# Kernel optimization log

Hardware: AMD Instinct MI355X
Metric: run time of the kernel (lower is better)

Reference implementation:

```python
import jax, jax.numpy as jnp
import numpy as np

N = 100000          # nodes
MUL = 64            # multiplicity of each irrep in input_1 (64x0e + 64x1o)
O0, O1M, O2M = 320, 128, 64   # output multiplicities: 320x0e + 128x1o + 64x1e
SQRT3 = float(np.sqrt(3.0))
SQRT6 = float(np.sqrt(6.0))
# e3nn path weights: sqrt(dim(ir_out) / sum_paths_to_out(mul1*mul2))
PW0 = float(1.0 / np.sqrt(2.0 * MUL))     # 0e: two paths, x = 128
PW1 = float(np.sqrt(3.0 / (2.0 * MUL)))   # 1o: two paths, x = 128
PW2 = float(np.sqrt(3.0 / MUL))           # 1e: one path,  x = 64


def setup_inputs() -> dict:
    key = jax.random.key(0)
    k = jax.random.split(key, 8)
    return {
        "input_1": jax.random.normal(k[0], (N, 4 * MUL), jnp.float32),  # 64x0e + 64x1o
        "input_2": jax.random.normal(k[1], (N, 4), jnp.float32),        # 1x0e + 1x1o
        "W_a0_o0": jax.random.normal(k[2], (MUL, O0), jnp.float32),     # 0e x 0e -> 0e
        "W_b1_o0": jax.random.normal(k[3], (MUL, O0), jnp.float32),     # 1o x 1o -> 0e
        "W_a1_o1": jax.random.normal(k[4], (MUL, O1M), jnp.float32),    # 0e x 1o -> 1o
        "W_b0_o1": jax.random.normal(k[5], (MUL, O1M), jnp.float32),    # 1o x 0e -> 1o
        "W_b1_o2": jax.random.normal(k[6], (MUL, O2M), jnp.float32),    # 1o x 1o -> 1e
        "bias": jnp.zeros((O0,), jnp.float32),                          # on the 0e scalars
    }


def reference(input_1, input_2, W_a0_o0, W_b1_o0, W_a1_o1, W_b0_o1, W_b1_o2, bias):
    n = input_1.shape[0]
    s_a = input_1[:, :MUL]                        # [N, MUL]      0e block
    v_b = input_1[:, MUL:].reshape(n, MUL, 3)     # [N, MUL, 3]   1o block
    s0 = input_2[:, :1]                           # [N, 1]        0e attr
    v1 = input_2[:, 1:]                           # [N, 3]        1o attr

    # --- 0e output: (0e*0e) and (1o.1o)/sqrt3 (CG delta_ij/sqrt3), fully-connected weights
    dot_b1 = jnp.einsum('nuk,nk->nu', v_b, v1)    # [N, MUL]
    o0 = PW0 * ((s_a * s0) @ W_a0_o0 + (dot_b1 / SQRT3) @ W_b1_o0) + bias  # [N, O0]

    # --- 1o output: (0e x 1o) and (1o x 0e), CG delta/sqrt3
    o1 = (PW1 / SQRT3) * (
        jnp.einsum('nu,uw->nw', s_a, W_a1_o1)[:, :, None] * v1[:, None, :]
        + jnp.einsum('nuk,uw->nwk', v_b, W_b0_o1) * s0[:, :, None]
    )                                             # [N, O1M, 3]

    # --- 1e output: (1o x 1o), CG eps_ijk/sqrt6 -> cross product
    cr = jnp.cross(v_b, v1[:, None, :])           # [N, MUL, 3]
    o2 = (PW2 / SQRT6) * jnp.einsum('nuk,uw->nwk', cr, W_b1_o2)  # [N, O2M, 3]

    return jnp.concatenate([o0, o1.reshape(n, -1), o2.reshape(n, -1)], axis=-1)  # [N, 896]
```

## Files before the change

kernel.cpp:

```cpp
#include <hip/hip_runtime.h>


typedef __bf16 v8bf __attribute__((ext_vector_type(8)));
typedef float f32x4 __attribute__((ext_vector_type(4)));

#define PW0f   0.08838834764831845f
#define PW0S3f 0.05103103630798288f


__global__ __launch_bounds__(256) void prep_weights(
    const float* __restrict__ Wa0, const float* __restrict__ Wb1o0,
    const float* __restrict__ Wa1, const float* __restrict__ Wb0,
    const float* __restrict__ Wo2, unsigned short* __restrict__ ws) {
  int t = blockIdx.x * 256 + threadIdx.x;
  float v;
  int k, n, KS, base;
  if (t < 40960) {
    k = t / 320; n = t % 320; KS = 4; base = 0;
    v = (k < 64) ? Wa0[k * 320 + n] * PW0f : Wb1o0[(k - 64) * 320 + n] * PW0S3f;
  } else if (t < 49152) {
    int tt = t - 40960; k = tt / 128; n = tt % 128; KS = 2; base = 40960;
    v = Wa1[k * 128 + n] * PW0f;
  } else if (t < 57344) {
    int tt = t - 49152; k = tt / 128; n = tt % 128; KS = 2; base = 49152;
    v = Wb0[k * 128 + n] * PW0f;
  } else if (t < 61440) {
    int tt = t - 57344; k = tt / 64; n = tt % 64; KS = 2; base = 57344;
    v = Wo2[k * 64 + n] * PW0f;
  } else {
    return;
  }
  int nt = n >> 4, cc = n & 15, ks = k >> 5, qq = (k >> 3) & 3, j = k & 7;
  int addr = base + ((nt * KS + ks) * 64 + qq * 16 + cc) * 8 + j;
  __bf16 h = (__bf16)v;
  ws[addr] = __builtin_bit_cast(unsigned short, h);
}

__device__ __forceinline__ int fidx(int k, int m) {
  return (((k >> 5) * 64 + ((k >> 3) & 3) * 16 + m) * 8) + (k & 7);
}

__global__ __launch_bounds__(256) void tp_main(
    const float* __restrict__ in1, const float* __restrict__ in2,
    const float* __restrict__ bias, const unsigned short* __restrict__ wsb,
    float* __restrict__ out, int N) {
  __shared__ __attribute__((aligned(16))) float raw[16 * 256];
  __shared__ __attribute__((aligned(16))) float s0v1[16 * 4];
  __shared__ __attribute__((aligned(16))) __bf16 f0[2048];
  __shared__ __attribute__((aligned(16))) __bf16 fsa[1024];
  __shared__ __attribute__((aligned(16))) __bf16 fvb[3][1024];
  __shared__ __attribute__((aligned(16))) __bf16 fcr[3][1024];

  const int tid = threadIdx.x;
  const int r0 = blockIdx.x * 16;

  if (tid < 64) {
    int m = tid >> 2, cmp = tid & 3;
    int rr = r0 + m; if (rr >= N) rr = N - 1;
    s0v1[tid] = in2[rr * 4 + cmp];
  }
  for (int i = tid; i < 1024; i += 256) {
    int row = i >> 6, c4 = i & 63;
    int rr = r0 + row; if (rr >= N) rr = N - 1;
    const float4 v = *(const float4*)(in1 + (size_t)rr * 256 + c4 * 4);
    *(float4*)(raw + row * 256 + c4 * 4) = v;
  }
  __syncthreads();

  {
    const int m = tid >> 4;
    const float s0  = s0v1[m * 4 + 0];
    const float v1x = s0v1[m * 4 + 1];
    const float v1y = s0v1[m * 4 + 2];
    const float v1z = s0v1[m * 4 + 3];
#pragma unroll
    for (int du = 0; du < 4; ++du) {
      const int u = (tid & 15) * 4 + du;
      const float sa = raw[m * 256 + u];
      const float b0 = raw[m * 256 + 64 + 3 * u + 0];
      const float b1 = raw[m * 256 + 64 + 3 * u + 1];
      const float b2 = raw[m * 256 + 64 + 3 * u + 2];
      f0[fidx(u, m)]      = (__bf16)(sa * s0);
      f0[fidx(64 + u, m)] = (__bf16)(b0 * v1x + b1 * v1y + b2 * v1z);
      fsa[fidx(u, m)]     = (__bf16)sa;
      fvb[0][fidx(u, m)]  = (__bf16)b0;
      fvb[1][fidx(u, m)]  = (__bf16)b1;
      fvb[2][fidx(u, m)]  = (__bf16)b2;
      fcr[0][fidx(u, m)]  = (__bf16)(b1 * v1z - b2 * v1y);
      fcr[1][fidx(u, m)]  = (__bf16)(b2 * v1x - b0 * v1z);
      fcr[2][fidx(u, m)]  = (__bf16)(b0 * v1y - b1 * v1x);
    }
  }
  __syncthreads();

  const int lane = tid & 63;
  const int wv = tid >> 6;
  const int c = lane & 15, q = lane >> 4;

  const unsigned short* B0p = wsb;
  const unsigned short* Ba1 = wsb + 40960;
  const unsigned short* Bb0 = wsb + 49152;
  const unsigned short* Bo2 = wsb + 57344;

  for (int job = wv; job < 32; job += 4) {
    if (job < 20) {
      const int nt = job;
      f32x4 acc = {0.f, 0.f, 0.f, 0.f};
#pragma unroll
      for (int ks = 0; ks < 4; ++ks) {
        v8bf a = *(const v8bf*)(f0 + (ks * 64 + lane) * 8);
        v8bf b = *(const v8bf*)(B0p + ((nt * 4 + ks) * 64 + lane) * 8);
        acc = __builtin_amdgcn_mfma_f32_16x16x32_bf16(a, b, acc, 0, 0, 0);
      }
      const int col = nt * 16 + c;
      const float bv = bias[col];
#pragma unroll
      for (int r = 0; r < 4; ++r) {
        const int row = r0 + q * 4 + r;
        if (row < N) out[(size_t)row * 896 + col] = acc[r] + bv;
      }
    } else if (job < 28) {
      const int jt = job - 20;
      f32x4 t1 = {0.f, 0.f, 0.f, 0.f};
      f32x4 t2[3];
      t2[0] = t1; t2[1] = t1; t2[2] = t1;
      v8bf ba0 = *(const v8bf*)(Ba1 + ((jt * 2 + 0) * 64 + lane) * 8);
      v8bf ba1 = *(const v8bf*)(Ba1 + ((jt * 2 + 1) * 64 + lane) * 8);
      v8bf bb0 = *(const v8bf*)(Bb0 + ((jt * 2 + 0) * 64 + lane) * 8);
      v8bf bb1 = *(const v8bf*)(Bb0 + ((jt * 2 + 1) * 64 + lane) * 8);
      {
        v8bf a0 = *(const v8bf*)(fsa + (0 * 64 + lane) * 8);
        v8bf a1 = *(const v8bf*)(fsa + (1 * 64 + lane) * 8);
        t1 = __builtin_amdgcn_mfma_f32_16x16x32_bf16(a0, ba0, t1, 0, 0, 0);
        t1 = __builtin_amdgcn_mfma_f32_16x16x32_bf16(a1, ba1, t1, 0, 0, 0);
      }
#pragma unroll
      for (int k = 0; k < 3; ++k) {
        v8bf a0 = *(const v8bf*)(fvb[k] + (0 * 64 + lane) * 8);
        v8bf a1 = *(const v8bf*)(fvb[k] + (1 * 64 + lane) * 8);
        t2[k] = __builtin_amdgcn_mfma_f32_16x16x32_bf16(a0, bb0, t2[k], 0, 0, 0);
        t2[k] = __builtin_amdgcn_mfma_f32_16x16x32_bf16(a1, bb1, t2[k], 0, 0, 0);
      }
#pragma unroll
      for (int r = 0; r < 4; ++r) {
        const int row = q * 4 + r;
        const int gr = r0 + row;
        if (gr < N) {
          const float s0  = s0v1[row * 4 + 0];
          const float v1x = s0v1[row * 4 + 1];
          const float v1y = s0v1[row * 4 + 2];
          const float v1z = s0v1[row * 4 + 3];
          const size_t base = (size_t)gr * 896 + 320 + 3 * (jt * 16 + c);
          out[base + 0] = t1[r] * v1x + t2[0][r] * s0;
          out[base + 1] = t1[r] * v1y + t2[1][r] * s0;
          out[base + 2] = t1[r] * v1z + t2[2][r] * s0;
        }
      }
    } else {
      const int jt = job - 28;
      f32x4 ac[3];
      ac[0] = f32x4{0.f, 0.f, 0.f, 0.f}; ac[1] = ac[0]; ac[2] = ac[0];
      v8bf b0v = *(const v8bf*)(Bo2 + ((jt * 2 + 0) * 64 + lane) * 8);
      v8bf b1v = *(const v8bf*)(Bo2 + ((jt * 2 + 1) * 64 + lane) * 8);
#pragma unroll
      for (int k = 0; k < 3; ++k) {
        v8bf a0 = *(const v8bf*)(fcr[k] + (0 * 64 + lane) * 8);
        v8bf a1 = *(const v8bf*)(fcr[k] + (1 * 64 + lane) * 8);
        ac[k] = __builtin_amdgcn_mfma_f32_16x16x32_bf16(a0, b0v, ac[k], 0, 0, 0);
        ac[k] = __builtin_amdgcn_mfma_f32_16x16x32_bf16(a1, b1v, ac[k], 0, 0, 0);
      }
#pragma unroll
      for (int r = 0; r < 4; ++r) {
        const int row = q * 4 + r;
        const int gr = r0 + row;
        if (gr < N) {
          const size_t base = (size_t)gr * 896 + 704 + 3 * (jt * 16 + c);
          out[base + 0] = ac[0][r];
          out[base + 1] = ac[1][r];
          out[base + 2] = ac[2][r];
        }
      }
    }
  }
}

extern "C" void kernel_launch(void* const* d_in, const int* in_sizes, int n_in,
                              void* d_out, int out_size, void* d_ws, size_t ws_size,
                              hipStream_t stream) {
  const float* in1   = (const float*)d_in[0];
  const float* in2   = (const float*)d_in[1];
  const float* Wa0   = (const float*)d_in[2];
  const float* Wb1o0 = (const float*)d_in[3];
  const float* Wa1   = (const float*)d_in[4];
  const float* Wb0   = (const float*)d_in[5];
  const float* Wo2   = (const float*)d_in[6];
  const float* bias  = (const float*)d_in[7];
  float* out = (float*)d_out;
  unsigned short* ws = (unsigned short*)d_ws;

  const int N = in_sizes[0] / 256;

  hipLaunchKernelGGL(prep_weights, dim3(240), dim3(256), 0, stream,
                     Wa0, Wb1o0, Wa1, Wb0, Wo2, ws);
  const int nblocks = (N + 15) / 16;
  hipLaunchKernelGGL(tp_main, dim3(nblocks), dim3(256), 0, stream,
                     in1, in2, bias, ws, out, N);
}
```

Measured before the change: 469.7 us.

## Apply per-row attribute scalars after MFMA instead of building product features

The per-row scalars (s0, v1) are factored out of the matmuls, so the MFMAs run directly on raw sa and vb features and the dot, cross and scale are applied to the accumulators in the epilogue. This removes the staging buffer of raw fp32 input and the f0/fcr feature arrays from shared memory, and the global loads now feed bf16 packing directly as vector stores. A-operand fragments are loaded into registers once and reused across all jobs, and launch bounds request higher occupancy. In exchange, the 0e output path needs more MFMAs (4 accumulators instead of 1), and the epilogue does more FLOPs.

```diff
diff --git a/kernel.cpp b/kernel.cpp
--- a/kernel.cpp
+++ b/kernel.cpp
@@ -2,6 +2,7 @@
 
 
 typedef __bf16 v8bf __attribute__((ext_vector_type(8)));
+typedef __bf16 v4bf __attribute__((ext_vector_type(4)));
 typedef float f32x4 __attribute__((ext_vector_type(4)));
 
 #define PW0f   0.08838834764831845f
@@ -13,82 +14,59 @@
     const float* __restrict__ Wa1, const float* __restrict__ Wb0,
     const float* __restrict__ Wo2, unsigned short* __restrict__ ws) {
   int t = blockIdx.x * 256 + threadIdx.x;
-  float v;
-  int k, n, KS, base;
-  if (t < 40960) {
-    k = t / 320; n = t % 320; KS = 4; base = 0;
-    v = (k < 64) ? Wa0[k * 320 + n] * PW0f : Wb1o0[(k - 64) * 320 + n] * PW0S3f;
+  float v; int k, n, base;
+  if (t < 20480) {
+    k = t / 320; n = t % 320; base = 0;     v = Wa0[k * 320 + n] * PW0f;
+  } else if (t < 40960) {
+    int tt = t - 20480; k = tt / 320; n = tt % 320; base = 20480; v = Wb1o0[k * 320 + n] * PW0S3f;
   } else if (t < 49152) {
-    int tt = t - 40960; k = tt / 128; n = tt % 128; KS = 2; base = 40960;
-    v = Wa1[k * 128 + n] * PW0f;
+    int tt = t - 40960; k = tt / 128; n = tt % 128; base = 40960; v = Wa1[k * 128 + n] * PW0f;
   } else if (t < 57344) {
-    int tt = t - 49152; k = tt / 128; n = tt % 128; KS = 2; base = 49152;
-    v = Wb0[k * 128 + n] * PW0f;
-  } else if (t < 61440) {
-    int tt = t - 57344; k = tt / 64; n = tt % 64; KS = 2; base = 57344;
-    v = Wo2[k * 64 + n] * PW0f;
+    int tt = t - 49152; k = tt / 128; n = tt % 128; base = 49152; v = Wb0[k * 128 + n] * PW0f;
   } else {
-    return;
+    int tt = t - 57344; k = tt / 64;  n = tt % 64;  base = 57344; v = Wo2[k * 64 + n] * PW0f;
   }
   int nt = n >> 4, cc = n & 15, ks = k >> 5, qq = (k >> 3) & 3, j = k & 7;
-  int addr = base + ((nt * KS + ks) * 64 + qq * 16 + cc) * 8 + j;
+  int addr = base + ((nt * 2 + ks) * 64 + qq * 16 + cc) * 8 + j;
   __bf16 h = (__bf16)v;
   ws[addr] = __builtin_bit_cast(unsigned short, h);
 }
 
-__device__ __forceinline__ int fidx(int k, int m) {
-  return (((k >> 5) * 64 + ((k >> 3) & 3) * 16 + m) * 8) + (k & 7);
-}
-
-__global__ __launch_bounds__(256) void tp_main(
+__global__ __launch_bounds__(256, 4) void tp_main(
     const float* __restrict__ in1, const float* __restrict__ in2,
     const float* __restrict__ bias, const unsigned short* __restrict__ wsb,
     float* __restrict__ out, int N) {
-  __shared__ __attribute__((aligned(16))) float raw[16 * 256];
   __shared__ __attribute__((aligned(16))) float s0v1[16 * 4];
-  __shared__ __attribute__((aligned(16))) __bf16 f0[2048];
   __shared__ __attribute__((aligned(16))) __bf16 fsa[1024];
   __shared__ __attribute__((aligned(16))) __bf16 fvb[3][1024];
-  __shared__ __attribute__((aligned(16))) __bf16 fcr[3][1024];
 
   const int tid = threadIdx.x;
   const int r0 = blockIdx.x * 16;
 
-  if (tid < 64) {
-    int m = tid >> 2, cmp = tid & 3;
+  {
+    const int m = tid & 15;
+    const int g = tid >> 4;
     int rr = r0 + m; if (rr >= N) rr = N - 1;
-    s0v1[tid] = in2[rr * 4 + cmp];
-  }
-  for (int i = tid; i < 1024; i += 256) {
-    int row = i >> 6, c4 = i & 63;
-    int rr = r0 + row; if (rr >= N) rr = N - 1;
-    const float4 v = *(const float4*)(in1 + (size_t)rr * 256 + c4 * 4);
-    *(float4*)(raw + row * 256 + c4 * 4) = v;
-  }
-  __syncthreads();
-
-  {
-    const int m = tid >> 4;
-    const float s0  = s0v1[m * 4 + 0];
-    const float v1x = s0v1[m * 4 + 1];
-    const float v1y = s0v1[m * 4 + 2];
-    const float v1z = s0v1[m * 4 + 3];
+    const float* rp = in1 + (size_t)rr * 256;
+    const float4 sa4 = *(const float4*)(rp + 4 * g);
+    const float4 w0  = *(const float4*)(rp + 64 + 12 * g);
+    const float4 w1  = *(const float4*)(rp + 64 + 12 * g + 4);
+    const float4 w2  = *(const float4*)(rp + 64 + 12 * g + 8);
+    const float vf[12] = {w0.x, w0.y, w0.z, w0.w, w1.x, w1.y, w1.z, w1.w,
+                          w2.x, w2.y, w2.z, w2.w};
+    const int wbase = (((g >> 3) * 64 + ((g >> 1) & 3) * 16 + m) * 8) + 4 * (g & 1);
+    v4bf pk;
+    pk[0] = (__bf16)sa4.x; pk[1] = (__bf16)sa4.y; pk[2] = (__bf16)sa4.z; pk[3] = (__bf16)sa4.w;
+    *(v4bf*)(fsa + wbase) = pk;
 #pragma unroll
-    for (int du = 0; du < 4; ++du) {
-      const int u = (tid & 15) * 4 + du;
-      const float sa = raw[m * 256 + u];
-      const float b0 = raw[m * 256 + 64 + 3 * u + 0];
-      const float b1 = raw[m * 256 + 64 + 3 * u + 1];
-      const float b2 = raw[m * 256 + 64 + 3 * u + 2];
-      f0[fidx(u, m)]      = (__bf16)(sa * s0);
-      f0[fidx(64 + u, m)] = (__bf16)(b0 * v1x + b1 * v1y + b2 * v1z);
-      fsa[fidx(u, m)]     = (__bf16)sa;
-      fvb[0][fidx(u, m)]  = (__bf16)b0;
-      fvb[1][fidx(u, m)]  = (__bf16)b1;
-      fvb[2][fidx(u, m)]  = (__bf16)b2;
-      fcr[0][fidx(u, m)]  = (__bf16)(b1 * v1z - b2 * v1y);
-      fcr[1][fidx(u, m)]  = (__bf16)(b2 * v1x - b0 * v1z);
-      fcr[2][fidx(u, m)]  = (__bf16)(b0 * v1y - b1 * v1x);
+    for (int c3 = 0; c3 < 3; ++c3) {
+      pk[0] = (__bf16)vf[c3]; pk[1] = (__bf16)vf[3 + c3];
+      pk[2] = (__bf16)vf[6 + c3]; pk[3] = (__bf16)vf[9 + c3];
+      *(v4bf*)(fvb[c3] + wbase) = pk;
+    }
+    if (tid < 16) {
+      int rr2 = r0 + tid; if (rr2 >= N) rr2 = N - 1;
+      *(float4*)(s0v1 + tid * 4) = *(const float4*)(in2 + (size_t)rr2 * 4);
     }
   }
   __syncthreads();
@@ -97,87 +75,93 @@
   const int wv = tid >> 6;
   const int c = lane & 15, q = lane >> 4;
 
-  const unsigned short* B0p = wsb;
-  const unsigned short* Ba1 = wsb + 40960;
-  const unsigned short* Bb0 = wsb + 49152;
-  const unsigned short* Bo2 = wsb + 57344;
+  v8bf a_sa[2], a_vb[3][2];
+#pragma unroll
+  for (int ks = 0; ks < 2; ++ks) {
+    a_sa[ks] = *(const v8bf*)(fsa + (ks * 64 + lane) * 8);
+#pragma unroll
+    for (int c3 = 0; c3 < 3; ++c3)
+      a_vb[c3][ks] = *(const v8bf*)(fvb[c3] + (ks * 64 + lane) * 8);
+  }
+  float4 sv[4];
+#pragma unroll
+  for (int r = 0; r < 4; ++r) sv[r] = *(const float4*)(s0v1 + (q * 4 + r) * 4);
+
+  const unsigned short* Wa0p = wsb;
+  const unsigned short* Wb1p = wsb + 20480;
+  const unsigned short* Wa1p = wsb + 40960;
+  const unsigned short* Wb0p = wsb + 49152;
+  const unsigned short* Wo2p = wsb + 57344;
 
   for (int job = wv; job < 32; job += 4) {
     if (job < 20) {
       const int nt = job;
-      f32x4 acc = {0.f, 0.f, 0.f, 0.f};
+      v8bf wa0 = *(const v8bf*)(Wa0p + ((nt * 2 + 0) * 64 + lane) * 8);
+      v8bf wa1 = *(const v8bf*)(Wa0p + ((nt * 2 + 1) * 64 + lane) * 8);
+      v8bf wb0 = *(const v8bf*)(Wb1p + ((nt * 2 + 0) * 64 + lane) * 8);
+      v8bf wb1 = *(const v8bf*)(Wb1p + ((nt * 2 + 1) * 64 + lane) * 8);
+      f32x4 ta = {0.f, 0.f, 0.f, 0.f};
+      f32x4 tb[3]; tb[0] = ta; tb[1] = ta; tb[2] = ta;
+      ta = __builtin_amdgcn_mfma_f32_16x16x32_bf16(a_sa[0], wa0, ta, 0, 0, 0);
+      ta = __builtin_amdgcn_mfma_f32_16x16x32_bf16(a_sa[1], wa1, ta, 0, 0, 0);
 #pragma unroll
-      for (int ks = 0; ks < 4; ++ks) {
-        v8bf a = *(const v8bf*)(f0 + (ks * 64 + lane) * 8);
-        v8bf b = *(const v8bf*)(B0p + ((nt * 4 + ks) * 64 + lane) * 8);
-        acc = __builtin_amdgcn_mfma_f32_16x16x32_bf16(a, b, acc, 0, 0, 0);
+      for (int c3 = 0; c3 < 3; ++c3) {
+        tb[c3] = __builtin_amdgcn_mfma_f32_16x16x32_bf16(a_vb[c3][0], wb0, tb[c3], 0, 0, 0);
+        tb[c3] = __builtin_amdgcn_mfma_f32_16x16x32_bf16(a_vb[c3][1], wb1, tb[c3], 0, 0, 0);
       }
       const int col = nt * 16 + c;
       const float bv = bias[col];
 #pragma unroll
       for (int r = 0; r < 4; ++r) {
-        const int row = r0 + q * 4 + r;
-        if (row < N) out[(size_t)row * 896 + col] = acc[r] + bv;
+        const int gr = r0 + q * 4 + r;
+        if (gr < N)
+          out[(size_t)gr * 896 + col] =
+              bv + sv[r].x * ta[r] + sv[r].y * tb[0][r] + sv[r].z * tb[1][r] + sv[r].w * tb[2][r];
       }
     } else if (job < 28) {
       const int jt = job - 20;
+      v8bf ba0 = *(const v8bf*)(Wa1p + ((jt * 2 + 0) * 64 + lane) * 8);
+      v8bf ba1 = *(const v8bf*)(Wa1p + ((jt * 2 + 1) * 64 + lane) * 8);
+      v8bf bb0 = *(const v8bf*)(Wb0p + ((jt * 2 + 0) * 64 + lane) * 8);
+      v8bf bb1 = *(const v8bf*)(Wb0p + ((jt * 2 + 1) * 64 + lane) * 8);
       f32x4 t1 = {0.f, 0.f, 0.f, 0.f};
-      f32x4 t2[3];
-      t2[0] = t1; t2[1] = t1; t2[2] = t1;
-      v8bf ba0 = *(const v8bf*)(Ba1 + ((jt * 2 + 0) * 64 + lane) * 8);
-      v8bf ba1 = *(const v8bf*)(Ba1 + ((jt * 2 + 1) * 64 + lane) * 8);
-      v8bf bb0 = *(const v8bf*)(Bb0 + ((jt * 2 + 0) * 64 + lane) * 8);
-      v8bf bb1 = *(const v8bf*)(Bb0 + ((jt * 2 + 1) * 64 + lane) * 8);
-      {
-        v8bf a0 = *(const v8bf*)(fsa + (0 * 64 + lane) * 8);
-        v8bf a1 = *(const v8bf*)(fsa + (1 * 64 + lane) * 8);
-        t1 = __builtin_amdgcn_mfma_f32_16x16x32_bf16(a0, ba0, t1, 0, 0, 0);
-        t1 = __builtin_amdgcn_mfma_f32_16x16x32_bf16(a1, ba1, t1, 0, 0, 0);
-      }
+      f32x4 t2[3]; t2[0] = t1; t2[1] = t1; t2[2] = t1;
+      t1 = __builtin_amdgcn_mfma_f32_16x16x32_bf16(a_sa[0], ba0, t1, 0, 0, 0);
+      t1 = __builtin_amdgcn_mfma_f32_16x16x32_bf16(a_sa[1], ba1, t1, 0, 0, 0);
 #pragma unroll
-      for (int k = 0; k < 3; ++k) {
-        v8bf a0 = *(const v8bf*)(fvb[k] + (0 * 64 + lane) * 8);
-        v8bf a1 = *(const v8bf*)(fvb[k] + (1 * 64 + lane) * 8);
-        t2[k] = __builtin_amdgcn_mfma_f32_16x16x32_bf16(a0, bb0, t2[k], 0, 0, 0);
-        t2[k] = __builtin_amdgcn_mfma_f32_16x16x32_bf16(a1, bb1, t2[k], 0, 0, 0);
+      for (int c3 = 0; c3 < 3; ++c3) {
+        t2[c3] = __builtin_amdgcn_mfma_f32_16x16x32_bf16(a_vb[c3][0], bb0, t2[c3], 0, 0, 0);
+        t2[c3] = __builtin_amdgcn_mfma_f32_16x16x32_bf16(a_vb[c3][1], bb1, t2[c3], 0, 0, 0);
       }
 #pragma unroll
       for (int r = 0; r < 4; ++r) {
-        const int row = q * 4 + r;
-        const int gr = r0 + row;
+        const int gr = r0 + q * 4 + r;
         if (gr < N) {
-          const float s0  = s0v1[row * 4 + 0];
-          const float v1x = s0v1[row * 4 + 1];
-          const float v1y = s0v1[row * 4 + 2];
-          const float v1z = s0v1[row * 4 + 3];
           const size_t base = (size_t)gr * 896 + 320 + 3 * (jt * 16 + c);
-          out[base + 0] = t1[r] * v1x + t2[0][r] * s0;
-          out[base + 1] = t1[r] * v1y + t2[1][r] * s0;
-          out[base + 2] = t1[r] * v1z + t2[2][r] * s0;
+          out[base + 0] = t1[r] * sv[r].y + t2[0][r] * sv[r].x;
+          out[base + 1] = t1[r] * sv[r].z + t2[1][r] * sv[r].x;
+          out[base + 2] = t1[r] * sv[r].w + t2[2][r] * sv[r].x;
         }
       }
     } else {
       const int jt = job - 28;
-      f32x4 ac[3];
-      ac[0] = f32x4{0.f, 0.f, 0.f, 0.f}; ac[1] = ac[0]; ac[2] = ac[0];
-      v8bf b0v = *(const v8bf*)(Bo2 + ((jt * 2 + 0) * 64 + lane) * 8);
-      v8bf b1v = *(const v8bf*)(Bo2 + ((jt * 2 + 1) * 64 + lane) * 8);
+      v8bf b0v = *(const v8bf*)(Wo2p + ((jt * 2 + 0) * 64 + lane) * 8);
+      v8bf b1v = *(const v8bf*)(Wo2p + ((jt * 2 + 1) * 64 + lane) * 8);
+      f32x4 t3[3];
+      t3[0] = f32x4{0.f, 0.f, 0.f, 0.f}; t3[1] = t3[0]; t3[2] = t3[0];
 #pragma unroll
-      for (int k = 0; k < 3; ++k) {
-        v8bf a0 = *(const v8bf*)(fcr[k] + (0 * 64 + lane) * 8);
-        v8bf a1 = *(const v8bf*)(fcr[k] + (1 * 64 + lane) * 8);
-        ac[k] = __builtin_amdgcn_mfma_f32_16x16x32_bf16(a0, b0v, ac[k], 0, 0, 0);
-        ac[k] = __builtin_amdgcn_mfma_f32_16x16x32_bf16(a1, b1v, ac[k], 0, 0, 0);
+      for (int c3 = 0; c3 < 3; ++c3) {
+        t3[c3] = __builtin_amdgcn_mfma_f32_16x16x32_bf16(a_vb[c3][0], b0v, t3[c3], 0, 0, 0);
+        t3[c3] = __builtin_amdgcn_mfma_f32_16x16x32_bf16(a_vb[c3][1], b1v, t3[c3], 0, 0, 0);
       }
 #pragma unroll
       for (int r = 0; r < 4; ++r) {
-        const int row = q * 4 + r;
-        const int gr = r0 + row;
+        const int gr = r0 + q * 4 + r;
         if (gr < N) {
           const size_t base = (size_t)gr * 896 + 704 + 3 * (jt * 16 + c);
-          out[base + 0] = ac[0][r];
-          out[base + 1] = ac[1][r];
-          out[base + 2] = ac[2][r];
+          out[base + 0] = t3[1][r] * sv[r].w - t3[2][r] * sv[r].z;
+          out[base + 1] = t3[2][r] * sv[r].y - t3[0][r] * sv[r].w;
+          out[base + 2] = t3[0][r] * sv[r].z - t3[1][r] * sv[r].y;
         }
       }
     }
```

Result: faster. 454.0 us (-3.4%).
